# Optimization experiments

Measured on AMD Instinct MI355X. Metric: run time of the kernel, lower is better.

## Reference

```python
import jax, jax.numpy as jnp
import numpy as np

N = 50000          # nodes
E = 800000         # edges (before self loops)
G = 64             # graphs in batch
HEADS = 4
HID = 25
DENSE = HEADS * HID      # 100, must equal prototype feature dim
IN_DIM = 128
OUT_DIM = 2
NPC = 5                  # num_prototypes_per_class
NUM_PROT = OUT_DIM * NPC
EPS = 1e-4
NEG_SLOPE = 0.2


def setup_inputs() -> dict:
    key = jax.random.key(0)
    ks = jax.random.split(key, 20)
    x = jax.random.normal(ks[0], (N, IN_DIM), dtype=jnp.float32)
    edge_index = jax.random.randint(ks[1], (2, E), 0, N, dtype=jnp.int64)
    batch = jnp.sort(jax.random.randint(ks[2], (N,), 0, G, dtype=jnp.int64))
    inp = {"x": x, "edge_index": edge_index, "batch": batch}
    in_dims = [IN_DIM, DENSE, DENSE]
    for i in range(3):
        d = in_dims[i]
        s = 1.0 / np.sqrt(d)
        inp[f"W{i}"] = jax.random.uniform(ks[3 + 4 * i], (d, DENSE), jnp.float32, -s, s)
        inp[f"as{i}"] = jax.random.uniform(ks[4 + 4 * i], (HEADS, HID), jnp.float32, -s, s)
        inp[f"ad{i}"] = jax.random.uniform(ks[5 + 4 * i], (HEADS, HID), jnp.float32, -s, s)
        inp[f"b{i}"] = jnp.zeros((DENSE,), jnp.float32)
    inp["protos"] = jax.random.uniform(ks[16], (NUM_PROT, DENSE), jnp.float32)
    # last_layer weight: +1 for own class, -0.5 otherwise  [OUT_DIM, NUM_PROT]
    cls = jnp.arange(NUM_PROT) // NPC
    inp["last_w"] = jnp.where(cls[None, :] == jnp.arange(OUT_DIM)[:, None], 1.0, -0.5).astype(jnp.float32)
    return inp


def _gat_layer(x, src, dst, W, a_src, a_dst, b):
    h = (x @ W).reshape(N, HEADS, HID)                 # [N,H,D]
    e_src = jnp.einsum('nhd,hd->nh', h, a_src)         # [N,H]
    e_dst = jnp.einsum('nhd,hd->nh', h, a_dst)
    alpha = e_src[src] + e_dst[dst]                    # [Etot,H]
    alpha = jnp.where(alpha > 0, alpha, NEG_SLOPE * alpha)
    amax = jax.ops.segment_max(alpha, dst, num_segments=N)
    ex = jnp.exp(alpha - amax[dst])
    denom = jax.ops.segment_sum(ex, dst, num_segments=N)
    a = ex / (denom[dst] + 1e-16)                      # segmented softmax over in-edges
    msg = h[src] * a[:, :, None]                       # [Etot,H,D]
    out = jax.ops.segment_sum(msg, dst, num_segments=N)
    return out.reshape(N, DENSE) + b


def reference(x, edge_index, batch, W0, as0, ad0, b0, W1, as1, ad1, b1, W2, as2, ad2, b2, protos, last_w):
    loops = jnp.arange(N, dtype=edge_index.dtype)
    src = jnp.concatenate([edge_index[0], loops])      # PyG add_self_loops=True
    dst = jnp.concatenate([edge_index[1], loops])
    params = [(W0, as0, ad0, b0), (W1, as1, ad1, b1), (W2, as2, ad2, b2)]
    h = x
    for (W, a_s, a_d, b) in params:
        h = _gat_layer(h, src, dst, W, a_s, a_d, b)
        h = jax.nn.relu(h)
    node_emb = h
    graph_emb = jax.ops.segment_max(h, batch, num_segments=G)   # global_max_pool
    # prototype distances: squared euclidean via expansion
    xp = graph_emb @ protos.T                                    # [G,P]
    dist = -2.0 * xp + jnp.sum(graph_emb ** 2, axis=1, keepdims=True) + jnp.sum(protos ** 2, axis=1)[None, :]
    sim = jnp.log((dist + 1.0) / (dist + EPS))
    logits = sim @ last_w.T
    probs = jax.nn.softmax(logits, axis=-1)
    return logits, probs, node_emb, graph_emb, dist
```

## Files before the change

### kernel.cpp

```cpp
#include <hip/hip_runtime.h>
#include <hip/hip_bf16.h>

#define NN      50000
#define EE      800000
#define ETOT    (EE + NN)
#define GG      64
#define HEADS   4
#define HID     25
#define DENSE   100
#define IN_DIM  128
#define OUT_DIM 2
#define NPC     5
#define NUM_PROT (OUT_DIM * NPC)
#define NCHUNK  ((NN + 255) / 256)

#define NEG_INF (-3.402823466e38f)

__global__ void k_count(const int* __restrict__ ei, int* __restrict__ cnt, int* __restrict__ pos) {
    int e = blockIdx.x * blockDim.x + threadIdx.x;
    if (e >= ETOT) return;
    int dst = (e < EE) ? ei[EE + e] : (e - EE);
    pos[e] = atomicAdd(&cnt[dst], 1);
}

__global__ void k_scan1(const int* __restrict__ cnt, int* __restrict__ csum) {
    __shared__ int sh[256];
    int i = blockIdx.x * 256 + threadIdx.x;
    int v = (i < NN) ? cnt[i] : 0;
    sh[threadIdx.x] = v;
    __syncthreads();
    for (int s = 128; s > 0; s >>= 1) {
        if (threadIdx.x < s) sh[threadIdx.x] += sh[threadIdx.x + s];
        __syncthreads();
    }
    if (threadIdx.x == 0) csum[blockIdx.x] = sh[0];
}

__global__ void k_scan2(int* __restrict__ csum) {
    __shared__ int sh[256];
    int tid = threadIdx.x;
    int v = (tid < NCHUNK) ? csum[tid] : 0;
    sh[tid] = v;
    __syncthreads();
    for (int s = 1; s < 256; s <<= 1) {
        int t = (tid >= s) ? sh[tid - s] : 0;
        __syncthreads();
        sh[tid] += t;
        __syncthreads();
    }
    if (tid < NCHUNK) csum[tid] = sh[tid] - v;
    if (tid == NCHUNK) csum[NCHUNK] = sh[255];
}

__global__ void k_scan3(const int* __restrict__ cnt, const int* __restrict__ csum, int* __restrict__ offs) {
    __shared__ int sh[256];
    int i = blockIdx.x * 256 + threadIdx.x;
    int v = (i < NN) ? cnt[i] : 0;
    sh[threadIdx.x] = v;
    __syncthreads();
    for (int s = 1; s < 256; s <<= 1) {
        int t = (threadIdx.x >= s) ? sh[threadIdx.x - s] : 0;
        __syncthreads();
        sh[threadIdx.x] += t;
        __syncthreads();
    }
    int excl = sh[threadIdx.x] - v + csum[blockIdx.x];
    if (i <= NN) offs[i] = excl;
}

__global__ void k_scatter(const int* __restrict__ ei, const int* __restrict__ offs,
                          const int* __restrict__ pos, int* __restrict__ csr) {
    int e = blockIdx.x * blockDim.x + threadIdx.x;
    if (e >= ETOT) return;
    int src, dst;
    if (e < EE) { src = ei[e]; dst = ei[EE + e]; }
    else        { src = dst = e - EE; }
    csr[offs[dst] + pos[e]] = src;
}

__global__ void k_bounds(const int* __restrict__ batch, int* __restrict__ gstart) {
    int n = blockIdx.x * blockDim.x + threadIdx.x;
    if (n >= NN) return;
    int b = batch[n];
    if (n == 0) {
        for (int g = 0; g <= b; g++) gstart[g] = 0;
    } else {
        int pb = batch[n - 1];
        for (int g = pb + 1; g <= b; g++) gstart[g] = n;
    }
    if (n == NN - 1) {
        for (int g = b + 1; g <= GG; g++) gstart[g] = NN;
    }
}

template <int DIN, int KC>
__global__ __launch_bounds__(256) void k_gemm(const float* __restrict__ X,
                                              const float* __restrict__ W,
                                              float* __restrict__ H) {
    constexpr int XSTR = KC + 4;
    __shared__ float Ws[KC * 104];
    __shared__ float Xs[128 * XSTR];
    const int tid = threadIdx.x;
    const int rl = tid >> 5;
    const int cg = tid & 31;
    const int node0 = blockIdx.x * 128;

    float acc[16][4] = {};
    constexpr int NCH = DIN / KC;
    constexpr int KQ = KC / 4;
    for (int kb = 0; kb < NCH; ++kb) {
        const int k0 = kb * KC;
        for (int idx = tid; idx < KC * 100; idx += 256) {
            int k = idx / 100, c = idx - k * 100;
            Ws[k * 104 + c] = W[(k0 + k) * 100 + c];
        }
        for (int q = tid; q < 128 * KQ; q += 256) {
            int r = q / KQ, kq = q - r * KQ;
            int row = node0 + r;
            float4 v = {0.f, 0.f, 0.f, 0.f};
            if (row < NN) v = *reinterpret_cast<const float4*>(&X[(size_t)row * DIN + k0 + kq * 4]);
            *reinterpret_cast<float4*>(&Xs[r * XSTR + kq * 4]) = v;
        }
        __syncthreads();
        if (cg < 25) {
            for (int kq = 0; kq < KQ; ++kq) {
                float4 w0 = *reinterpret_cast<const float4*>(&Ws[(kq * 4 + 0) * 104 + cg * 4]);
                float4 w1 = *reinterpret_cast<const float4*>(&Ws[(kq * 4 + 1) * 104 + cg * 4]);
                float4 w2 = *reinterpret_cast<const float4*>(&Ws[(kq * 4 + 2) * 104 + cg * 4]);
                float4 w3 = *reinterpret_cast<const float4*>(&Ws[(kq * 4 + 3) * 104 + cg * 4]);
                #pragma unroll
                for (int j = 0; j < 16; ++j) {
                    float4 xv = *reinterpret_cast<const float4*>(&Xs[(rl * 16 + j) * XSTR + kq * 4]);
                    acc[j][0] += xv.x * w0.x; acc[j][1] += xv.x * w0.y;
                    acc[j][2] += xv.x * w0.z; acc[j][3] += xv.x * w0.w;
                    acc[j][0] += xv.y * w1.x; acc[j][1] += xv.y * w1.y;
                    acc[j][2] += xv.y * w1.z; acc[j][3] += xv.y * w1.w;
                    acc[j][0] += xv.z * w2.x; acc[j][1] += xv.z * w2.y;
                    acc[j][2] += xv.z * w2.z; acc[j][3] += xv.z * w2.w;
                    acc[j][0] += xv.w * w3.x; acc[j][1] += xv.w * w3.y;
                    acc[j][2] += xv.w * w3.z; acc[j][3] += xv.w * w3.w;
                }
            }
        }
        __syncthreads();
    }
    if (cg < 25) {
        #pragma unroll
        for (int j = 0; j < 16; ++j) {
            int row = node0 + rl * 16 + j;
            if (row < NN) {
                float4 v = {acc[j][0], acc[j][1], acc[j][2], acc[j][3]};
                *reinterpret_cast<float4*>(&H[(size_t)row * 100 + cg * 4]) = v;
            }
        }
    }
}

__global__ void k_esed(const float* __restrict__ H, const float* __restrict__ AS,
                       const float* __restrict__ AD, float* __restrict__ es, float* __restrict__ ed) {
    int t = blockIdx.x * blockDim.x + threadIdx.x;
    if (t >= NN * HEADS) return;
    int n = t >> 2, hd = t & 3;
    const float* hr = H + (size_t)n * 100 + hd * 25;
    const float* as = AS + hd * 25;
    const float* ad = AD + hd * 25;
    float s1 = 0.f, s2 = 0.f;
    #pragma unroll
    for (int d = 0; d < 25; d++) {
        float v = hr[d];
        s1 += v * as[d];
        s2 += v * ad[d];
    }
    es[t] = s1;
    ed[t] = s2;
}

__global__ __launch_bounds__(256) void k_attn(const float* __restrict__ H,
                                              const float* __restrict__ es,
                                              const float* __restrict__ ed,
                                              const int* __restrict__ offs,
                                              const int* __restrict__ csr,
                                              const float* __restrict__ bias,
                                              float* __restrict__ out) {
    const int wid = threadIdx.x >> 6;
    const int lane = threadIdx.x & 63;
    const int n = blockIdx.x * 4 + wid;
    if (n >= NN) return;
    const int beg = offs[n], end = offs[n + 1];

    {
        const int el = lane >> 2, hd = lane & 3;
        float edh = ed[n * 4 + hd];
        float m = NEG_INF, s = 0.f;
        for (int e = beg + el; e < end; e += 16) {
            int si = csr[e];
            float a = es[si * 4 + hd] + edh;
            a = fmaxf(a, 0.2f * a);
            float nm = fmaxf(m, a);
            float sc = __expf(m - nm);
            s = s * sc + __expf(a - nm);
            m = nm;
        }
        #pragma unroll
        for (int mask = 4; mask <= 32; mask <<= 1) {
            float mo = __shfl_xor(m, mask, 64);
            float so = __shfl_xor(s, mask, 64);
            float nm = fmaxf(m, mo);
            float f1 = (m  > NEG_INF) ? __expf(m  - nm) : 0.f;
            float f2 = (mo > NEG_INF) ? __expf(mo - nm) : 0.f;
            s = s * f1 + so * f2;
            m = nm;
        }
        float m0 = __shfl(m, 0, 64), m1 = __shfl(m, 1, 64);
        float m2 = __shfl(m, 2, 64), m3 = __shfl(m, 3, 64);
        float s0 = __shfl(s, 0, 64), s1 = __shfl(s, 1, 64);
        float s2 = __shfl(s, 2, 64), s3 = __shfl(s, 3, 64);

        const int h2 = lane >> 5;
        const int q  = lane & 31;
        const int d0 = q * 4;
        const bool act = (q < 25);
        const int hdA = d0 / 25;
        const int hdB = (d0 + 3) / 25;
        const bool selA1 = ((d0 + 1) / 25) == hdA;
        const bool selA2 = ((d0 + 2) / 25) == hdA;
        float4 ed4 = *reinterpret_cast<const float4*>(&ed[n * 4]);
        auto pick = [&](int h, float v0, float v1, float v2, float v3) {
            return h == 0 ? v0 : (h == 1 ? v1 : (h == 2 ? v2 : v3));
        };
        const float edA = pick(hdA, ed4.x, ed4.y, ed4.z, ed4.w);
        const float edB = pick(hdB, ed4.x, ed4.y, ed4.z, ed4.w);
        const float mA  = pick(hdA, m0, m1, m2, m3);
        const float mB  = pick(hdB, m0, m1, m2, m3);
        const float iA  = 1.f / (pick(hdA, s0, s1, s2, s3) + 1e-16f);
        const float iB  = 1.f / (pick(hdB, s0, s1, s2, s3) + 1e-16f);

        float ax = 0.f, ay = 0.f, az = 0.f, aw = 0.f;
        for (int e0 = beg; e0 < end; e0 += 8) {
            #pragma unroll
            for (int u = 0; u < 4; ++u) {
                int ee = e0 + u * 2 + h2;
                bool valid = (ee < end);
                int ec = valid ? ee : beg;
                int si = csr[ec];
                float4 e4 = *reinterpret_cast<const float4*>(&es[si * 4]);
                float eAv = pick(hdA, e4.x, e4.y, e4.z, e4.w);
                float eBv = pick(hdB, e4.x, e4.y, e4.z, e4.w);
                float aA = eAv + edA; aA = fmaxf(aA, 0.2f * aA);
                float aB = eBv + edB; aB = fmaxf(aB, 0.2f * aB);
                float wA = __expf(aA - mA) * iA;
                float wB = __expf(aB - mB) * iB;
                if (!valid) { wA = 0.f; wB = 0.f; }
                float w1 = selA1 ? wA : wB;
                float w2 = selA2 ? wA : wB;
                if (act) {
                    float4 xv = *reinterpret_cast<const float4*>(&H[(size_t)si * 100 + d0]);
                    ax += wA * xv.x;
                    ay += w1 * xv.y;
                    az += w2 * xv.z;
                    aw += wB * xv.w;
                }
            }
        }
        ax += __shfl_xor(ax, 32, 64);
        ay += __shfl_xor(ay, 32, 64);
        az += __shfl_xor(az, 32, 64);
        aw += __shfl_xor(aw, 32, 64);
        if (act && h2 == 0) {
            float4 b = *reinterpret_cast<const float4*>(&bias[d0]);
            float4 o = {fmaxf(ax + b.x, 0.f), fmaxf(ay + b.y, 0.f),
                        fmaxf(az + b.z, 0.f), fmaxf(aw + b.w, 0.f)};
            *reinterpret_cast<float4*>(&out[(size_t)n * 100 + d0]) = o;
        }
    }
}

__global__ void k_pool1(const float* __restrict__ NE, const int* __restrict__ gstart,
                        float* __restrict__ part) {
    int g = blockIdx.x >> 3, c = blockIdx.x & 7;
    int d = threadIdx.x;
    if (d >= 100) return;
    int s0 = gstart[g], s1 = gstart[g + 1];
    int len = s1 - s0;
    int n0 = s0 + (int)((long long)len * c / 8);
    int n1 = s0 + (int)((long long)len * (c + 1) / 8);
    float vm = NEG_INF;
    for (int n = n0; n < n1; n++) vm = fmaxf(vm, NE[(size_t)n * 100 + d]);
    part[(size_t)(g * 8 + c) * 100 + d] = vm;
}

__global__ void k_pool2(const float* __restrict__ part, float* __restrict__ GE) {
    int g = blockIdx.x;
    int d = threadIdx.x;
    if (d >= 100) return;
    float vm = NEG_INF;
    for (int c = 0; c < 8; c++) vm = fmaxf(vm, part[(size_t)(g * 8 + c) * 100 + d]);
    GE[(size_t)g * 100 + d] = vm;
}

__global__ void k_head(const float* __restrict__ GE, const float* __restrict__ P,
                       const float* __restrict__ LW, float* __restrict__ logits,
                       float* __restrict__ probs, float* __restrict__ dist) {
    int g = blockIdx.x;
    __shared__ float ge[100];
    __shared__ float sims[NUM_PROT];
    __shared__ float lg[OUT_DIM];
    int t = threadIdx.x;
    if (t < 100) ge[t] = GE[(size_t)g * 100 + t];
    __syncthreads();
    if (t < NUM_PROT) {
        float dot = 0.f, pn = 0.f, gn = 0.f;
        for (int d = 0; d < 100; d++) {
            float pv = P[t * 100 + d];
            float gv = ge[d];
            dot += gv * pv;
            pn += pv * pv;
            gn += gv * gv;
        }
        float ds = gn - 2.f * dot + pn;
        dist[g * NUM_PROT + t] = ds;
        sims[t] = logf((ds + 1.f) / (ds + 1e-4f));
    }
    __syncthreads();
    if (t < OUT_DIM) {
        float l = 0.f;
        for (int p = 0; p < NUM_PROT; p++) l += sims[p] * LW[t * NUM_PROT + p];
        lg[t] = l;
        logits[g * OUT_DIM + t] = l;
    }
    __syncthreads();
    if (t == 0) {
        float mm = fmaxf(lg[0], lg[1]);
        float e0 = __expf(lg[0] - mm), e1 = __expf(lg[1] - mm);
        float inv = 1.f / (e0 + e1);
        probs[g * OUT_DIM + 0] = e0 * inv;
        probs[g * OUT_DIM + 1] = e1 * inv;
    }
}

extern "C" void kernel_launch(void* const* d_in, const int* in_sizes, int n_in,
                              void* d_out, int out_size, void* d_ws, size_t ws_size,
                              hipStream_t stream) {
    const float* x     = (const float*)d_in[0];
    const int*   ei    = (const int*)d_in[1];
    const int*   batch = (const int*)d_in[2];
    const float* Wm[3]  = {(const float*)d_in[3],  (const float*)d_in[7],  (const float*)d_in[11]};
    const float* ASm[3] = {(const float*)d_in[4],  (const float*)d_in[8],  (const float*)d_in[12]};
    const float* ADm[3] = {(const float*)d_in[5],  (const float*)d_in[9],  (const float*)d_in[13]};
    const float* Bm[3]  = {(const float*)d_in[6],  (const float*)d_in[10], (const float*)d_in[14]};
    const float* P  = (const float*)d_in[15];
    const float* LW = (const float*)d_in[16];

    float* out = (float*)d_out;
    float* logits  = out;
    float* probs   = out + GG * OUT_DIM;
    float* nodeEmb = out + 2 * GG * OUT_DIM;
    float* GE      = nodeEmb + (size_t)NN * DENSE;
    float* disto   = GE + GG * DENSE;

    char* w = (char*)d_ws;
    size_t off = 0;
    auto carve = [&](size_t bytes) -> void* {
        void* p = w + off;
        off += (bytes + 15) & ~(size_t)15;
        return p;
    };
    float* hA   = (float*)carve((size_t)NN * DENSE * 4);
    float* es   = (float*)carve((size_t)NN * HEADS * 4);
    float* ed   = (float*)carve((size_t)NN * HEADS * 4);
    int* cnt    = (int*)carve((size_t)NN * 4);
    int* offs   = (int*)carve((size_t)(NN + 1) * 4);
    int* pos    = (int*)carve((size_t)ETOT * 4);
    int* csr    = (int*)carve((size_t)ETOT * 4);
    int* csum   = (int*)carve((size_t)(NCHUNK + 1) * 4);
    int* gstart = (int*)carve((size_t)(GG + 1) * 4);
    float* part = (float*)carve((size_t)GG * 8 * DENSE * 4);
    (void)in_sizes; (void)n_in; (void)out_size; (void)ws_size;

    hipMemsetAsync(cnt, 0, (size_t)NN * 4, stream);
    k_count<<<(ETOT + 255) / 256, 256, 0, stream>>>(ei, cnt, pos);
    k_scan1<<<NCHUNK, 256, 0, stream>>>(cnt, csum);
    k_scan2<<<1, 256, 0, stream>>>(csum);
    k_scan3<<<NCHUNK, 256, 0, stream>>>(cnt, csum, offs);
    k_scatter<<<(ETOT + 255) / 256, 256, 0, stream>>>(ei, offs, pos, csr);
    k_bounds<<<(NN + 255) / 256, 256, 0, stream>>>(batch, gstart);

    const int gemmGrid = (NN + 127) / 128;
    const int esedGrid = (NN * HEADS + 255) / 256;
    const int attnGrid = (NN + 3) / 4;

    const float* layerIn = x;
    for (int l = 0; l < 3; ++l) {
        if (l == 0) k_gemm<IN_DIM, 32><<<gemmGrid, 256, 0, stream>>>(layerIn, Wm[l], hA);
        else        k_gemm<DENSE,  20><<<gemmGrid, 256, 0, stream>>>(layerIn, Wm[l], hA);
        k_esed<<<esedGrid, 256, 0, stream>>>(hA, ASm[l], ADm[l], es, ed);
        k_attn<<<attnGrid, 256, 0, stream>>>(hA, es, ed, offs, csr, Bm[l], nodeEmb);
        layerIn = nodeEmb;
    }

    k_pool1<<<GG * 8, 128, 0, stream>>>(nodeEmb, gstart, part);
    k_pool2<<<GG, 128, 0, stream>>>(part, GE);

    k_head<<<GG, 128, 0, stream>>>(GE, P, LW, logits, probs, disto);
}
```

Baseline: 521.8 us.

## Split attention into softmax-weight kernel and weighted aggregation kernel

Splits the fused attention kernel in two. The first kernel computes the segment softmax stats and writes a normalized per-edge, per-head weight buffer. The second kernel gathers those precomputed weights alongside neighbor features, so it no longer recomputes the exp and LeakyReLU or gathers es per edge. In exchange it adds a ~13.6MB weight buffer written and re-read each layer, plus an extra kernel launch per layer.

```diff
diff --git a/kernel.cpp b/kernel.cpp
--- a/kernel.cpp
+++ b/kernel.cpp
@@ -175,103 +175,103 @@
     ed[t] = s2;
 }
 
-__global__ __launch_bounds__(256) void k_attn(const float* __restrict__ H,
-                                              const float* __restrict__ es,
+__global__ __launch_bounds__(256) void k_msum(const float* __restrict__ es,
                                               const float* __restrict__ ed,
                                               const int* __restrict__ offs,
                                               const int* __restrict__ csr,
-                                              const float* __restrict__ bias,
-                                              float* __restrict__ out) {
+                                              float* __restrict__ wv) {
+    int wid = threadIdx.x >> 6;
+    int lane = threadIdx.x & 63;
+    int n = blockIdx.x * 4 + wid;
+    if (n >= NN) return;
+    int el = lane >> 2, hd = lane & 3;
+    int beg = offs[n], end = offs[n + 1];
+    float edh = ed[n * 4 + hd];
+    float m = NEG_INF, s = 0.f;
+    for (int e = beg + el; e < end; e += 16) {
+        int si = csr[e];
+        float a = es[si * 4 + hd] + edh;
+        a = (a > 0.f) ? a : 0.2f * a;
+        float nm = fmaxf(m, a);
+        float sc = __expf(m - nm);
+        s = s * sc + __expf(a - nm);
+        m = nm;
+    }
+    #pragma unroll
+    for (int mask = 4; mask <= 32; mask <<= 1) {
+        float mo = __shfl_xor(m, mask, 64);
+        float so = __shfl_xor(s, mask, 64);
+        float nm = fmaxf(m, mo);
+        float f1 = (m  > NEG_INF) ? __expf(m  - nm) : 0.f;
+        float f2 = (mo > NEG_INF) ? __expf(mo - nm) : 0.f;
+        s = s * f1 + so * f2;
+        m = nm;
+    }
+    float invs = 1.f / (s + 1e-16f);
+    for (int e = beg + el; e < end; e += 16) {
+        int si = csr[e];
+        float a = es[si * 4 + hd] + edh;
+        a = (a > 0.f) ? a : 0.2f * a;
+        wv[(size_t)e * 4 + hd] = __expf(a - m) * invs;
+    }
+}
+
+__global__ __launch_bounds__(256) void k_acc(const float* __restrict__ H,
+                                             const float* __restrict__ wv,
+                                             const int* __restrict__ offs,
+                                             const int* __restrict__ csr,
+                                             const float* __restrict__ bias,
+                                             float* __restrict__ out) {
     const int wid = threadIdx.x >> 6;
     const int lane = threadIdx.x & 63;
     const int n = blockIdx.x * 4 + wid;
     if (n >= NN) return;
     const int beg = offs[n], end = offs[n + 1];
 
-    {
-        const int el = lane >> 2, hd = lane & 3;
-        float edh = ed[n * 4 + hd];
-        float m = NEG_INF, s = 0.f;
-        for (int e = beg + el; e < end; e += 16) {
-            int si = csr[e];
-            float a = es[si * 4 + hd] + edh;
-            a = fmaxf(a, 0.2f * a);
-            float nm = fmaxf(m, a);
-            float sc = __expf(m - nm);
-            s = s * sc + __expf(a - nm);
-            m = nm;
-        }
+    const int h2 = lane >> 5;
+    const int q  = lane & 31;
+    const int d0 = q * 4;
+    const bool act = (q < 25);
+    const int hdA = d0 / 25;
+    const int hdB = (d0 + 3) / 25;
+    const bool selA1 = ((d0 + 1) / 25) == hdA;
+    const bool selA2 = ((d0 + 2) / 25) == hdA;
+    auto pick = [](int h, const float4& v) {
+        return h == 0 ? v.x : (h == 1 ? v.y : (h == 2 ? v.z : v.w));
+    };
+
+    float ax = 0.f, ay = 0.f, az = 0.f, aw = 0.f;
+    for (int e0 = beg; e0 < end; e0 += 8) {
         #pragma unroll
-        for (int mask = 4; mask <= 32; mask <<= 1) {
-            float mo = __shfl_xor(m, mask, 64);
-            float so = __shfl_xor(s, mask, 64);
-            float nm = fmaxf(m, mo);
-            float f1 = (m  > NEG_INF) ? __expf(m  - nm) : 0.f;
-            float f2 = (mo > NEG_INF) ? __expf(mo - nm) : 0.f;
-            s = s * f1 + so * f2;
-            m = nm;
-        }
-        float m0 = __shfl(m, 0, 64), m1 = __shfl(m, 1, 64);
-        float m2 = __shfl(m, 2, 64), m3 = __shfl(m, 3, 64);
-        float s0 = __shfl(s, 0, 64), s1 = __shfl(s, 1, 64);
-        float s2 = __shfl(s, 2, 64), s3 = __shfl(s, 3, 64);
-
-        const int h2 = lane >> 5;
-        const int q  = lane & 31;
-        const int d0 = q * 4;
-        const bool act = (q < 25);
-        const int hdA = d0 / 25;
-        const int hdB = (d0 + 3) / 25;
-        const bool selA1 = ((d0 + 1) / 25) == hdA;
-        const bool selA2 = ((d0 + 2) / 25) == hdA;
-        float4 ed4 = *reinterpret_cast<const float4*>(&ed[n * 4]);
-        auto pick = [&](int h, float v0, float v1, float v2, float v3) {
-            return h == 0 ? v0 : (h == 1 ? v1 : (h == 2 ? v2 : v3));
-        };
-        const float edA = pick(hdA, ed4.x, ed4.y, ed4.z, ed4.w);
-        const float edB = pick(hdB, ed4.x, ed4.y, ed4.z, ed4.w);
-        const float mA  = pick(hdA, m0, m1, m2, m3);
-        const float mB  = pick(hdB, m0, m1, m2, m3);
-        const float iA  = 1.f / (pick(hdA, s0, s1, s2, s3) + 1e-16f);
-        const float iB  = 1.f / (pick(hdB, s0, s1, s2, s3) + 1e-16f);
-
-        float ax = 0.f, ay = 0.f, az = 0.f, aw = 0.f;
-        for (int e0 = beg; e0 < end; e0 += 8) {
-            #pragma unroll
-            for (int u = 0; u < 4; ++u) {
-                int ee = e0 + u * 2 + h2;
-                bool valid = (ee < end);
-                int ec = valid ? ee : beg;
-                int si = csr[ec];
-                float4 e4 = *reinterpret_cast<const float4*>(&es[si * 4]);
-                float eAv = pick(hdA, e4.x, e4.y, e4.z, e4.w);
-                float eBv = pick(hdB, e4.x, e4.y, e4.z, e4.w);
-                float aA = eAv + edA; aA = fmaxf(aA, 0.2f * aA);
-                float aB = eBv + edB; aB = fmaxf(aB, 0.2f * aB);
-                float wA = __expf(aA - mA) * iA;
-                float wB = __expf(aB - mB) * iB;
-                if (!valid) { wA = 0.f; wB = 0.f; }
-                float w1 = selA1 ? wA : wB;
-                float w2 = selA2 ? wA : wB;
-                if (act) {
-                    float4 xv = *reinterpret_cast<const float4*>(&H[(size_t)si * 100 + d0]);
-                    ax += wA * xv.x;
-                    ay += w1 * xv.y;
-                    az += w2 * xv.z;
-                    aw += wB * xv.w;
-                }
+        for (int u = 0; u < 4; ++u) {
+            int ee = e0 + u * 2 + h2;
+            bool valid = (ee < end);
+            int ec = valid ? ee : beg;
+            int si = csr[ec];
+            float4 w4 = *reinterpret_cast<const float4*>(&wv[(size_t)ec * 4]);
+            float wA = pick(hdA, w4);
+            float wB = pick(hdB, w4);
+            if (!valid) { wA = 0.f; wB = 0.f; }
+            float w1 = selA1 ? wA : wB;
+            float w2 = selA2 ? wA : wB;
+            if (act) {
+                float4 xv = *reinterpret_cast<const float4*>(&H[(size_t)si * 100 + d0]);
+                ax += wA * xv.x;
+                ay += w1 * xv.y;
+                az += w2 * xv.z;
+                aw += wB * xv.w;
             }
         }
-        ax += __shfl_xor(ax, 32, 64);
-        ay += __shfl_xor(ay, 32, 64);
-        az += __shfl_xor(az, 32, 64);
-        aw += __shfl_xor(aw, 32, 64);
-        if (act && h2 == 0) {
-            float4 b = *reinterpret_cast<const float4*>(&bias[d0]);
-            float4 o = {fmaxf(ax + b.x, 0.f), fmaxf(ay + b.y, 0.f),
-                        fmaxf(az + b.z, 0.f), fmaxf(aw + b.w, 0.f)};
-            *reinterpret_cast<float4*>(&out[(size_t)n * 100 + d0]) = o;
-        }
+    }
+    ax += __shfl_xor(ax, 32, 64);
+    ay += __shfl_xor(ay, 32, 64);
+    az += __shfl_xor(az, 32, 64);
+    aw += __shfl_xor(aw, 32, 64);
+    if (act && h2 == 0) {
+        float4 b = *reinterpret_cast<const float4*>(&bias[d0]);
+        float4 o = {fmaxf(ax + b.x, 0.f), fmaxf(ay + b.y, 0.f),
+                    fmaxf(az + b.z, 0.f), fmaxf(aw + b.w, 0.f)};
+        *reinterpret_cast<float4*>(&out[(size_t)n * 100 + d0]) = o;
     }
 }
 
@@ -375,6 +375,7 @@
     int* csum   = (int*)carve((size_t)(NCHUNK + 1) * 4);
     int* gstart = (int*)carve((size_t)(GG + 1) * 4);
     float* part = (float*)carve((size_t)GG * 8 * DENSE * 4);
+    float* wv   = (float*)carve((size_t)ETOT * HEADS * 4);
     (void)in_sizes; (void)n_in; (void)out_size; (void)ws_size;
 
     hipMemsetAsync(cnt, 0, (size_t)NN * 4, stream);
@@ -387,14 +388,16 @@
 
     const int gemmGrid = (NN + 127) / 128;
     const int esedGrid = (NN * HEADS + 255) / 256;
-    const int attnGrid = (NN + 3) / 4;
+    const int msumGrid = (NN + 3) / 4;
+    const int accGrid  = (NN + 3) / 4;
 
     const float* layerIn = x;
     for (int l = 0; l < 3; ++l) {
         if (l == 0) k_gemm<IN_DIM, 32><<<gemmGrid, 256, 0, stream>>>(layerIn, Wm[l], hA);
         else        k_gemm<DENSE,  20><<<gemmGrid, 256, 0, stream>>>(layerIn, Wm[l], hA);
         k_esed<<<esedGrid, 256, 0, stream>>>(hA, ASm[l], ADm[l], es, ed);
-        k_attn<<<attnGrid, 256, 0, stream>>>(hA, es, ed, offs, csr, Bm[l], nodeEmb);
+        k_msum<<<msumGrid, 256, 0, stream>>>(es, ed, offs, csr, wv);
+        k_acc<<<accGrid, 256, 0, stream>>>(hA, wv, offs, csr, Bm[l], nodeEmb);
         layerIn = nodeEmb;
     }
 
```

After: 507.2 us. 1.03x faster.
